# Kernel optimization log

Measured on AMD Instinct MI355X. Metric: run time of the kernel, lower is better.

The kernel has to match this reference:

```python
import jax, jax.numpy as jnp
import numpy as np

B, L, D = 64, 512, 128  # batch, word_len, dim


def setup_inputs() -> dict:
    key = jax.random.key(0)
    ks = jax.random.split(key, 12)
    p = lambda k, s: jax.random.normal(k, s, dtype=jnp.float32) * 0.05
    return {
        "EW": jax.random.normal(ks[0], (B, L, D), dtype=jnp.float32),
        "ES": jax.random.normal(ks[1], (B, L, D), dtype=jnp.float32),
        "WQ_w": p(ks[2], (D, D)), "WQ_b": p(ks[3], (D,)),
        "WK_w": p(ks[4], (D, D)), "WK_b": p(ks[5], (D,)),
        "UQ_w": p(ks[6], (D, D)), "UQ_b": p(ks[7], (D,)),
        "UK_w": p(ks[8], (D, D)), "UK_b": p(ks[9], (D,)),
        "V_w": p(ks[10], (D, D)), "V_b": p(ks[11], (D,)),
    }


def reference(EW, ES, WQ_w, WQ_b, WK_w, WK_b, UQ_w, UQ_b, UK_w, UK_b, V_w, V_b):
    dim = EW.shape[-1]
    word_len = EW.shape[-2]
    scale = 1.0 / (2.0 * dim ** 0.5)
    # word-level Q/K and sentence-level UQ/UK projections (torch Linear: x @ W.T + b)
    Q = (EW @ WQ_w.T + WQ_b) * scale   # [B, L, D]
    K = (EW @ WK_w.T + WK_b) * scale   # [B, L, D]
    UQ = (ES @ UQ_w.T + UQ_b) * scale  # [B, L, D]
    UK = (ES @ UK_w.T + UK_b) * scale  # [B, L, D]
    # two-term score matrix [B, L, L]
    alpha = jnp.einsum('bid,bjd->bij', Q, K) + jnp.einsum('bid,bjd->bij', UQ, UK)
    # manual exp/sum softmax exactly as in the source (no max subtraction;
    # denominator is broadcast along axis 1, faithful to unsqueeze(1))
    numerator = jnp.exp(alpha)                      # [B, L, L]
    denominator = numerator.sum(axis=-1)[:, None, :]  # [B, 1, L]
    soft = numerator / denominator                  # [B, L, L]
    value = EW @ V_w.T + V_b                        # [B, L, D]
    # faithful reinterpreting view (NOT a transpose): [B, L, D] -> [B, D, L]
    value = value.reshape(-1, dim, word_len)
    result = value @ soft                           # [B, D, L]
    return result.reshape(-1, word_len, dim)        # [B, L, D]
```

## Files before the change

### kernel.cpp

```cpp
#include <hip/hip_runtime.h>
#include <hip/hip_bf16.h>

#define NB 64
#define NL 512
#define ND 128
#define NK 256

typedef unsigned short ush;
typedef __attribute__((ext_vector_type(8))) short short8;
typedef __attribute__((ext_vector_type(16))) float f32x16;


__device__ __forceinline__ ush f2bs(float f) {
    union { __hip_bfloat16 h; ush u; } cv;
    cv.h = __float2bfloat16(f);
    return cv.u;
}
__device__ __forceinline__ short8 pack_bf8(float4 a, float4 b) {
    short8 r;
    r[0] = (short)f2bs(a.x); r[1] = (short)f2bs(a.y);
    r[2] = (short)f2bs(a.z); r[3] = (short)f2bs(a.w);
    r[4] = (short)f2bs(b.x); r[5] = (short)f2bs(b.y);
    r[6] = (short)f2bs(b.z); r[7] = (short)f2bs(b.w);
    return r;
}
__device__ __forceinline__ f32x16 zero16() {
    f32x16 z = {0.f,0.f,0.f,0.f,0.f,0.f,0.f,0.f,0.f,0.f,0.f,0.f,0.f,0.f,0.f,0.f};
    return z;
}

__global__ __launch_bounds__(256) void wconv_kernel(
    const float* __restrict__ W0, const float* __restrict__ W1,
    const float* __restrict__ W2, const float* __restrict__ W3,
    const float* __restrict__ W4, ush* __restrict__ Wb)
{
    const int m = blockIdx.y;
    const float* W = (m == 0) ? W0 : (m == 1) ? W1 : (m == 2) ? W2 : (m == 3) ? W3 : W4;
    const int e = (blockIdx.x * 256 + threadIdx.x) * 4;
    float4 v = *(const float4*)(W + e);
    ushort4 o;
    o.x = f2bs(v.x); o.y = f2bs(v.y); o.z = f2bs(v.z); o.w = f2bs(v.w);
    *(ushort4*)(Wb + m * 16384 + e) = o;
}

__global__ __launch_bounds__(256) void projqk_kernel(
    const float* __restrict__ EW, const float* __restrict__ ES,
    const ush* __restrict__ Wb,
    const float* __restrict__ b0, const float* __restrict__ b1,
    const float* __restrict__ b2, const float* __restrict__ b3,
    ush* __restrict__ QUf, ush* __restrict__ KUf)
{
    __shared__ ush Tls[4][2048];
    const int f = blockIdx.x;
    const int xcd = f & 7, loc = f >> 3;
    const int rt = xcd * 32 + (loc >> 2);
    const int m  = loc & 3;
    const int tid = threadIdx.x, w = tid >> 6, lane = tid & 63;
    const int l5 = lane & 31, hi = lane >> 5;
    const float* X = (m >= 2) ? ES : EW;
    const int rbase = rt * 128 + w * 32;

    const float* xr = X + (size_t)(rbase + l5) * ND + hi * 8;
    short8 af[8];
    #pragma unroll
    for (int ks = 0; ks < 8; ++ks)
        af[ks] = pack_bf8(*(const float4*)(xr + ks * 16),
                          *(const float4*)(xr + ks * 16 + 4));

    const ush* Wm = Wb + m * 16384;
    const float* Bp = (m == 0) ? b0 : (m == 1) ? b1 : (m == 2) ? b2 : b3;
    const float scl = 0.044194173824159216f;

    char* Tc = (char*)Tls[w];
    ush* dstf = (m == 0 || m == 2) ? QUf : KUf;
    const int ko = (m >= 2) ? 8 : 0;
    const int p_g = rt * 4 + w;

    #pragma unroll
    for (int pass = 0; pass < 2; ++pass) {
        f32x16 acc[2];
        acc[0] = zero16(); acc[1] = zero16();
        #pragma unroll
        for (int ks = 0; ks < 8; ++ks) {
            #pragma unroll
            for (int nbl = 0; nbl < 2; ++nbl) {
                const int nb = pass * 2 + nbl;
                short8 bf_ = *(const short8*)(Wm + (nb * 32 + l5) * 128 + ks * 16 + hi * 8);
                acc[nbl] = __builtin_amdgcn_mfma_f32_32x32x16_bf16(af[ks], bf_, acc[nbl], 0, 0, 0);
            }
        }
        #pragma unroll
        for (int nbl = 0; nbl < 2; ++nbl) {
            const int nb = pass * 2 + nbl;
            float bias = Bp[nb * 32 + l5];
            #pragma unroll
            for (int r6 = 0; r6 < 16; ++r6) {
                int row = (r6 & 3) + 8 * (r6 >> 2) + 4 * hi;
                int boff = row * 128 + (((nbl * 32 + l5) * 2) ^ ((row & 7) << 4));
                *(ush*)(Tc + boff) = f2bs((acc[nbl][r6] + bias) * scl);
            }
        }
        #pragma unroll
        for (int ks8 = 0; ks8 < 4; ++ks8) {
            int boff = l5 * 128 + ((ks8 * 32 + hi * 16) ^ ((l5 & 7) << 4));
            short8 v = *(const short8*)(Tc + boff);
            int ksg = ko + pass * 4 + ks8;
            *(short8*)(dstf + ((size_t)(p_g * 16 + ksg) * 64 + lane) * 8) = v;
        }
    }
}

__global__ __launch_bounds__(256) void projv_kernel(
    const float* __restrict__ EW, const ush* __restrict__ Wb,
    const float* __restrict__ b4, ush* __restrict__ Vbf)
{
    __shared__ ush lds[16384];
    const int f = blockIdx.x;
    const int rt = (f & 7) * 32 + (f >> 3);
    const int tid = threadIdx.x, w = tid >> 6, lane = tid & 63;
    const int l5 = lane & 31, hi = lane >> 5;
    const int rbase = rt * 128 + w * 32;

    const float* xr = EW + (size_t)(rbase + l5) * ND + hi * 8;
    short8 af[8];
    #pragma unroll
    for (int ks = 0; ks < 8; ++ks)
        af[ks] = pack_bf8(*(const float4*)(xr + ks * 16),
                          *(const float4*)(xr + ks * 16 + 4));

    const ush* Wm = Wb + 4 * 16384;
    f32x16 acc[4];
    acc[0] = zero16(); acc[1] = zero16(); acc[2] = zero16(); acc[3] = zero16();
    #pragma unroll
    for (int ks = 0; ks < 8; ++ks) {
        #pragma unroll
        for (int nb = 0; nb < 4; ++nb) {
            short8 bf_ = *(const short8*)(Wm + (nb * 32 + l5) * 128 + ks * 16 + hi * 8);
            acc[nb] = __builtin_amdgcn_mfma_f32_32x32x16_bf16(af[ks], bf_, acc[nb], 0, 0, 0);
        }
    }

    char* Lc = (char*)lds;
    #pragma unroll
    for (int nb = 0; nb < 4; ++nb) {
        float bias = b4[nb * 32 + l5];
        #pragma unroll
        for (int r6 = 0; r6 < 16; ++r6) {
            int row5 = (r6 & 3) + 8 * (r6 >> 2) + 4 * hi;
            int dl = w * 8 + (row5 >> 2);
            int lcol = (row5 & 3) * 128 + nb * 32 + l5;
            int boff = dl * 1024 + ((lcol * 2) ^ ((dl & 7) << 4));
            *(ush*)(Lc + boff) = f2bs(acc[nb][r6] + bias);
        }
    }
    __syncthreads();
    #pragma unroll
    for (int it = 0; it < 8; ++it) {
        int chunk = it * 256 + tid;
        int ks = chunk >> 6, ln = chunk & 63;
        int l5b = ln & 31, hib = ln >> 5;
        int boff = l5b * 1024 + ((ks * 32 + hib * 16) ^ ((l5b & 7) << 4));
        short8 v = *(const short8*)(Lc + boff);
        *(short8*)(Vbf + ((size_t)(rt * 32 + ks) * 64 + ln) * 8) = v;
    }
}

__global__ __launch_bounds__(256) void alpha_kernel(
    const ush* __restrict__ QUf, const ush* __restrict__ KUf,
    ush* __restrict__ Nf, float* __restrict__ dPart)
{
    __shared__ float red[4][2][16];
    __shared__ ush TlsA[4][2048];
    const int f = blockIdx.x;
    const int xcd = f & 7, loc = f >> 3;
    const int b  = xcd * 8 + (loc >> 5);
    const int rt = (loc >> 1) & 15;
    const int ch = loc & 1;
    const int tid = threadIdx.x, w = tid >> 6, lane = tid & 63;
    const int l5 = lane & 31, hi = lane >> 5;
    const ush* Qb = QUf + (size_t)b * 131072;
    const ush* Kb = KUf + (size_t)b * 131072;
    ush* Nfb = Nf + (size_t)b * 262144;

    const ush* qp = Qb + (size_t)rt * 8192 + lane * 8;
    const int cpg0 = ch * 8 + w * 2;

    f32x16 a0[2], a1[2];
    a0[0] = zero16(); a0[1] = zero16(); a1[0] = zero16(); a1[1] = zero16();
    #pragma unroll
    for (int ks = 0; ks < 16; ks += 2) {
        short8 aqa = *(const short8*)(qp + ks * 512);
        short8 aqb = *(const short8*)(qp + (ks + 1) * 512);
        #pragma unroll
        for (int cp = 0; cp < 2; ++cp) {
            const ush* kp = Kb + (size_t)((cpg0 + cp) * 16) * 512 + lane * 8;
            a0[cp] = __builtin_amdgcn_mfma_f32_32x32x16_bf16(aqa,
                         *(const short8*)(kp + ks * 512), a0[cp], 0, 0, 0);
            a1[cp] = __builtin_amdgcn_mfma_f32_32x32x16_bf16(aqb,
                         *(const short8*)(kp + (ks + 1) * 512), a1[cp], 0, 0, 0);
        }
    }

    float rs[16];
    #pragma unroll
    for (int r6 = 0; r6 < 16; ++r6) rs[r6] = 0.f;
    char* Tc = (char*)TlsA[w];
    #pragma unroll
    for (int cp = 0; cp < 2; ++cp) {
        const int cpg = cpg0 + cp;
        float e[16];
        #pragma unroll
        for (int r6 = 0; r6 < 16; ++r6) {
            e[r6] = __expf(a0[cp][r6] + a1[cp][r6]);
            rs[r6] += e[r6];
        }
        #pragma unroll
        for (int q = 0; q < 8; ++q) {
            int r6 = q * 2;
            int r = (r6 & 3) + 8 * (r6 >> 2) + 4 * hi;
            unsigned int pk = (unsigned int)f2bs(e[r6])
                            | ((unsigned int)f2bs(e[r6 + 1]) << 16);
            *(unsigned int*)(Tc + l5 * 128 + ((r * 2) ^ ((l5 & 7) << 4))) = pk;
        }
        #pragma unroll
        for (int ksl = 0; ksl < 2; ++ksl) {
            short8 v = *(const short8*)(Tc + l5 * 128 +
                           (((ksl * 16 + hi * 8) * 2) ^ ((l5 & 7) << 4)));
            int ksg = rt * 2 + ksl;
            *(short8*)(Nfb + ((size_t)(cpg * 32 + ksg) * 64 + lane) * 8) = v;
        }
    }

    #pragma unroll
    for (int mk = 1; mk <= 16; mk <<= 1)
        #pragma unroll
        for (int r6 = 0; r6 < 16; ++r6) rs[r6] += __shfl_xor(rs[r6], mk, 32);
    if (l5 == 0)
        #pragma unroll
        for (int r6 = 0; r6 < 16; ++r6) red[w][hi][r6] = rs[r6];
    __syncthreads();
    if (tid < 32) {
        int t = tid;
        int hh = (t >> 2) & 1, r6 = (t & 3) + 4 * (t >> 3);
        float s = red[0][hh][r6] + red[1][hh][r6] + red[2][hh][r6] + red[3][hh][r6];
        dPart[((size_t)b * 2 + ch) * NL + rt * 32 + t] = s;
    }
}

__global__ __launch_bounds__(256) void pv_kernel(
    const ush* __restrict__ Vbf, const ush* __restrict__ Nf,
    const float* __restrict__ dPart, float* __restrict__ out)
{
    const int f = blockIdx.x;
    const int xcd = f & 7, loc = f >> 3;
    const int b  = xcd * 8 + (loc >> 4);
    const int ct = loc & 15;
    const int tid = threadIdx.x, w = tid >> 6, lane = tid & 63;
    const int l5 = lane & 31, hi = lane >> 5;
    const ush* Vbb = Vbf + (size_t)b * 65536;
    const ush* Nfb = Nf + (size_t)b * 262144;
    const size_t obase = (size_t)b * (ND * NL);

    const ush* vp = Vbb + (size_t)w * 16384 + lane * 8;
    const ush* np = Nfb + (size_t)ct * 16384 + lane * 8;

    f32x16 acc0 = zero16(), acc1 = zero16();
    #pragma unroll
    for (int ks = 0; ks < 32; ks += 2) {
        acc0 = __builtin_amdgcn_mfma_f32_32x32x16_bf16(*(const short8*)(vp + ks * 512),
                   *(const short8*)(np + ks * 512), acc0, 0, 0, 0);
        acc1 = __builtin_amdgcn_mfma_f32_32x32x16_bf16(*(const short8*)(vp + (ks + 1) * 512),
                   *(const short8*)(np + (ks + 1) * 512), acc1, 0, 0, 0);
    }
    f32x16 acc = acc0 + acc1;
    const int c0 = ct * 32;
    float rd = 1.0f / (dPart[((size_t)b * 2 + 0) * NL + c0 + l5]
                     + dPart[((size_t)b * 2 + 1) * NL + c0 + l5]);
    #pragma unroll
    for (int r6 = 0; r6 < 16; ++r6) {
        int d = w * 32 + (r6 & 3) + 8 * (r6 >> 2) + 4 * hi;
        out[obase + (size_t)d * NL + c0 + l5] = acc[r6] * rd;
    }
}

__global__ __launch_bounds__(256) void fused_kernel(
    const ush* __restrict__ QUf, const ush* __restrict__ KUf,
    const ush* __restrict__ Vbf, float* __restrict__ out)
{
    __shared__ ush Pt2[32 * 136];
    __shared__ float red[128];
    __shared__ float rdenS[32];
    const int f = blockIdx.x;
    const int xcd = f & 7, loc = f >> 3;
    const int b  = xcd * 8 + (loc >> 4);
    const int ct = loc & 15, c0 = ct * 32;
    const int tid = threadIdx.x, w = tid >> 6, lane = tid & 63;
    const int l5 = lane & 31, hi = lane >> 5;
    const ush* Qb  = QUf + (size_t)b * 131072;
    const ush* Kb  = KUf + (size_t)b * 131072;
    const ush* Vbb = Vbf + (size_t)b * 65536;
    const size_t obase = (size_t)b * (ND * NL);

    {
        short8 aq[16];
        const ush* qp = Qb + (size_t)ct * 8192 + lane * 8;
        #pragma unroll
        for (int ks = 0; ks < 16; ++ks) aq[ks] = *(const short8*)(qp + ks * 512);
        float rs[16];
        #pragma unroll
        for (int r = 0; r < 16; ++r) rs[r] = 0.f;
        #pragma unroll
        for (int t = 0; t < 4; ++t) {
            const ush* kp = Kb + (size_t)(w * 4 + t) * 8192 + lane * 8;
            f32x16 a0 = zero16(), a1 = zero16();
            #pragma unroll
            for (int ks = 0; ks < 16; ks += 2) {
                a0 = __builtin_amdgcn_mfma_f32_32x32x16_bf16(aq[ks],     *(const short8*)(kp + ks * 512),       a0, 0, 0, 0);
                a1 = __builtin_amdgcn_mfma_f32_32x32x16_bf16(aq[ks + 1], *(const short8*)(kp + (ks + 1) * 512), a1, 0, 0, 0);
            }
            #pragma unroll
            for (int r = 0; r < 16; ++r) rs[r] += __expf(a0[r] + a1[r]);
        }
        #pragma unroll
        for (int mk = 1; mk <= 16; mk <<= 1)
            #pragma unroll
            for (int r = 0; r < 16; ++r) rs[r] += __shfl_xor(rs[r], mk, 32);
        if (l5 == 0)
            #pragma unroll
            for (int r = 0; r < 16; ++r) red[(w * 2 + hi) * 16 + r] = rs[r];
    }
    __syncthreads();
    if (tid < 32) {
        int c = tid;
        int h2 = (c >> 2) & 1, r = (c & 3) + 4 * (c >> 3);
        float s = 0.f;
        #pragma unroll
        for (int kh = 0; kh < 4; ++kh) s += red[(kh * 2 + h2) * 16 + r];
        rdenS[c] = 1.0f / s;
    }
    __syncthreads();

    const int p2 = w;
    const float rden = rdenS[l5];
    const ush* kp2 = Kb + (size_t)ct * 8192 + lane * 8;
    f32x16 oA = zero16(), oB = zero16();

    for (int it = 0; it < 4; ++it) {
        if (it) __syncthreads();
        const ush* qp2 = Qb + (size_t)(it * 4 + p2) * 8192 + lane * 8;
        f32x16 s0 = zero16(), s1 = zero16();
        #pragma unroll
        for (int ks = 0; ks < 16; ks += 2) {
            s0 = __builtin_amdgcn_mfma_f32_32x32x16_bf16(*(const short8*)(qp2 + ks * 512),
                                                         *(const short8*)(kp2 + ks * 512),       s0, 0, 0, 0);
            s1 = __builtin_amdgcn_mfma_f32_32x32x16_bf16(*(const short8*)(qp2 + (ks + 1) * 512),
                                                         *(const short8*)(kp2 + (ks + 1) * 512), s1, 0, 0, 0);
        }
        #pragma unroll
        for (int q = 0; q < 4; ++q) {
            ushort4 pv;
            pv.x = f2bs(__expf(s0[q * 4 + 0] + s1[q * 4 + 0]) * rden);
            pv.y = f2bs(__expf(s0[q * 4 + 1] + s1[q * 4 + 1]) * rden);
            pv.z = f2bs(__expf(s0[q * 4 + 2] + s1[q * 4 + 2]) * rden);
            pv.w = f2bs(__expf(s0[q * 4 + 3] + s1[q * 4 + 3]) * rden);
            int boff = l5 * 272 + (((p2 * 32 + q * 8 + hi * 4) * 2) ^ ((l5 & 7) << 4));
            *(ushort4*)((char*)Pt2 + boff) = pv;
        }
        __syncthreads();
        #pragma unroll
        for (int j = 0; j < 8; j += 2) {
            short8 va0 = *(const short8*)(Vbb + ((size_t)(p2 * 32 + it * 8 + j) * 64 + lane) * 8);
            short8 pb0 = *(const short8*)((char*)Pt2 + l5 * 272 + (((j * 16 + hi * 8) * 2) ^ ((l5 & 7) << 4)));
            oA = __builtin_amdgcn_mfma_f32_32x32x16_bf16(va0, pb0, oA, 0, 0, 0);
            short8 va1 = *(const short8*)(Vbb + ((size_t)(p2 * 32 + it * 8 + j + 1) * 64 + lane) * 8);
            short8 pb1 = *(const short8*)((char*)Pt2 + l5 * 272 + ((((j + 1) * 16 + hi * 8) * 2) ^ ((l5 & 7) << 4)));
            oB = __builtin_amdgcn_mfma_f32_32x32x16_bf16(va1, pb1, oB, 0, 0, 0);
        }
    }
    f32x16 oacc = oA + oB;
    #pragma unroll
    for (int r = 0; r < 16; ++r) {
        int d = p2 * 32 + (r & 3) + 8 * (r >> 2) + 4 * hi;
        out[obase + (size_t)d * NL + c0 + l5] = oacc[r];
    }
}

extern "C" void kernel_launch(void* const* d_in, const int* in_sizes, int n_in,
                              void* d_out, int out_size, void* d_ws, size_t ws_size,
                              hipStream_t stream)
{
    const float* EW   = (const float*)d_in[0];
    const float* ES   = (const float*)d_in[1];
    const float* WQ_w = (const float*)d_in[2];
    const float* WQ_b = (const float*)d_in[3];
    const float* WK_w = (const float*)d_in[4];
    const float* WK_b = (const float*)d_in[5];
    const float* UQ_w = (const float*)d_in[6];
    const float* UQ_b = (const float*)d_in[7];
    const float* UK_w = (const float*)d_in[8];
    const float* UK_b = (const float*)d_in[9];
    const float* V_w  = (const float*)d_in[10];
    const float* V_b  = (const float*)d_in[11];

    if (ws_size < (size_t)41 * 1024 * 1024) return;

    char* ws = (char*)d_ws;
    ush* QUf = (ush*)ws;
    ush* KUf = (ush*)(ws + (size_t)16 * 1024 * 1024);
    ush* Vbf = (ush*)(ws + (size_t)32 * 1024 * 1024);
    ush* Wb  = (ush*)(ws + (size_t)40 * 1024 * 1024);
    float* dPart = (float*)(ws + (size_t)40 * 1024 * 1024 + 512 * 1024);
    ush* Nf  = (ush*)(ws + (size_t)41 * 1024 * 1024);
    float* outp = (float*)d_out;

    wconv_kernel<<<dim3(16, 5), 256, 0, stream>>>(WQ_w, WK_w, UQ_w, UK_w, V_w, Wb);
    projqk_kernel<<<1024, 256, 0, stream>>>(EW, ES, Wb,
                                            WQ_b, WK_b, UQ_b, UK_b, QUf, KUf);
    projv_kernel<<<256, 256, 0, stream>>>(EW, Wb, V_b, Vbf);
    if (ws_size >= (size_t)74 * 1024 * 1024) {
        alpha_kernel<<<2048, 256, 0, stream>>>(QUf, KUf, Nf, dPart);
        pv_kernel<<<1024, 256, 0, stream>>>(Vbf, Nf, dPart, outp);
    } else {
        fused_kernel<<<1024, 256, 0, stream>>>(QUf, KUf, Vbf, outp);
    }
}
```

Measured before the change: 80.54 us.

## Store Q/K projections in FP8 and compute scores with FP8 MFMA

The projection kernel now writes Q/UQ and K/UK as FP8 (e4m3) rather than bf16. It uses a larger pre-scale and folds the remaining 1/256 factor into the exponent argument. The alpha kernel uses the fp8 32x32x16 MFMA with 8-byte operand loads. This halves the Q/K traffic and uses the faster fp8 matrix path. The cost is lower precision in the score matrix, which feeds an exponential without max subtraction and can amplify error. The fused fallback kernel is removed, and the launcher now requires the larger workspace.

```diff
diff --git a/kernel.cpp b/kernel.cpp
--- a/kernel.cpp
+++ b/kernel.cpp
@@ -15,6 +15,11 @@
     union { __hip_bfloat16 h; ush u; } cv;
     cv.h = __float2bfloat16(f);
     return cv.u;
+}
+__device__ __forceinline__ float bs2f(ush u) {
+    union { unsigned int i; float f; } cv;
+    cv.i = ((unsigned int)u) << 16;
+    return cv.f;
 }
 __device__ __forceinline__ short8 pack_bf8(float4 a, float4 b) {
     short8 r;
@@ -48,7 +53,7 @@
     const ush* __restrict__ Wb,
     const float* __restrict__ b0, const float* __restrict__ b1,
     const float* __restrict__ b2, const float* __restrict__ b3,
-    ush* __restrict__ QUf, ush* __restrict__ KUf)
+    char* __restrict__ QUf, char* __restrict__ KUf)
 {
     __shared__ ush Tls[4][2048];
     const int f = blockIdx.x;
@@ -69,10 +74,10 @@
 
     const ush* Wm = Wb + m * 16384;
     const float* Bp = (m == 0) ? b0 : (m == 1) ? b1 : (m == 2) ? b2 : b3;
-    const float scl = 0.044194173824159216f;
+    const float scl = 0.70710678118654752f;
 
     char* Tc = (char*)Tls[w];
-    ush* dstf = (m == 0 || m == 2) ? QUf : KUf;
+    char* dstf = (m == 0 || m == 2) ? QUf : KUf;
     const int ko = (m >= 2) ? 8 : 0;
     const int p_g = rt * 4 + w;
 
@@ -104,8 +109,16 @@
         for (int ks8 = 0; ks8 < 4; ++ks8) {
             int boff = l5 * 128 + ((ks8 * 32 + hi * 16) ^ ((l5 & 7) << 4));
             short8 v = *(const short8*)(Tc + boff);
+            float fv[8];
+            #pragma unroll
+            for (int e = 0; e < 8; ++e) fv[e] = bs2f((ush)v[e]);
+            int dw0 = __builtin_amdgcn_cvt_pk_fp8_f32(fv[0], fv[1], 0, 0);
+            dw0     = __builtin_amdgcn_cvt_pk_fp8_f32(fv[2], fv[3], dw0, 1);
+            int dw1 = __builtin_amdgcn_cvt_pk_fp8_f32(fv[4], fv[5], 0, 0);
+            dw1     = __builtin_amdgcn_cvt_pk_fp8_f32(fv[6], fv[7], dw1, 1);
             int ksg = ko + pass * 4 + ks8;
-            *(short8*)(dstf + ((size_t)(p_g * 16 + ksg) * 64 + lane) * 8) = v;
+            int2 st; st.x = dw0; st.y = dw1;
+            *(int2*)(dstf + ((size_t)(p_g * 16 + ksg) * 64 + lane) * 8) = st;
         }
     }
 }
@@ -166,7 +179,7 @@
 }
 
 __global__ __launch_bounds__(256) void alpha_kernel(
-    const ush* __restrict__ QUf, const ush* __restrict__ KUf,
+    const char* __restrict__ QUf, const char* __restrict__ KUf,
     ush* __restrict__ Nf, float* __restrict__ dPart)
 {
     __shared__ float red[4][2][16];
@@ -178,27 +191,29 @@
     const int ch = loc & 1;
     const int tid = threadIdx.x, w = tid >> 6, lane = tid & 63;
     const int l5 = lane & 31, hi = lane >> 5;
-    const ush* Qb = QUf + (size_t)b * 131072;
-    const ush* Kb = KUf + (size_t)b * 131072;
+    const char* Qb = QUf + (size_t)b * 131072;
+    const char* Kb = KUf + (size_t)b * 131072;
     ush* Nfb = Nf + (size_t)b * 262144;
 
-    const ush* qp = Qb + (size_t)rt * 8192 + lane * 8;
+    const char* qp = Qb + (size_t)rt * 8192 + lane * 8;
     const int cpg0 = ch * 8 + w * 2;
+    const char* kp0 = Kb + (size_t)(cpg0 + 0) * 8192 + lane * 8;
+    const char* kp1 = Kb + (size_t)(cpg0 + 1) * 8192 + lane * 8;
 
     f32x16 a0[2], a1[2];
     a0[0] = zero16(); a0[1] = zero16(); a1[0] = zero16(); a1[1] = zero16();
     #pragma unroll
     for (int ks = 0; ks < 16; ks += 2) {
-        short8 aqa = *(const short8*)(qp + ks * 512);
-        short8 aqb = *(const short8*)(qp + (ks + 1) * 512);
-        #pragma unroll
-        for (int cp = 0; cp < 2; ++cp) {
-            const ush* kp = Kb + (size_t)((cpg0 + cp) * 16) * 512 + lane * 8;
-            a0[cp] = __builtin_amdgcn_mfma_f32_32x32x16_bf16(aqa,
-                         *(const short8*)(kp + ks * 512), a0[cp], 0, 0, 0);
-            a1[cp] = __builtin_amdgcn_mfma_f32_32x32x16_bf16(aqb,
-                         *(const short8*)(kp + (ks + 1) * 512), a1[cp], 0, 0, 0);
-        }
+        long aqa = *(const long*)(qp + ks * 512);
+        long aqb = *(const long*)(qp + (ks + 1) * 512);
+        a0[0] = __builtin_amdgcn_mfma_f32_32x32x16_fp8_fp8(aqa,
+                    *(const long*)(kp0 + ks * 512), a0[0], 0, 0, 0);
+        a1[0] = __builtin_amdgcn_mfma_f32_32x32x16_fp8_fp8(aqb,
+                    *(const long*)(kp0 + (ks + 1) * 512), a1[0], 0, 0, 0);
+        a0[1] = __builtin_amdgcn_mfma_f32_32x32x16_fp8_fp8(aqa,
+                    *(const long*)(kp1 + ks * 512), a0[1], 0, 0, 0);
+        a1[1] = __builtin_amdgcn_mfma_f32_32x32x16_fp8_fp8(aqb,
+                    *(const long*)(kp1 + (ks + 1) * 512), a1[1], 0, 0, 0);
     }
 
     float rs[16];
@@ -211,7 +226,7 @@
         float e[16];
         #pragma unroll
         for (int r6 = 0; r6 < 16; ++r6) {
-            e[r6] = __expf(a0[cp][r6] + a1[cp][r6]);
+            e[r6] = __expf((a0[cp][r6] + a1[cp][r6]) * 0.00390625f);
             rs[r6] += e[r6];
         }
         #pragma unroll
@@ -280,108 +295,6 @@
     for (int r6 = 0; r6 < 16; ++r6) {
         int d = w * 32 + (r6 & 3) + 8 * (r6 >> 2) + 4 * hi;
         out[obase + (size_t)d * NL + c0 + l5] = acc[r6] * rd;
-    }
-}
-
-__global__ __launch_bounds__(256) void fused_kernel(
-    const ush* __restrict__ QUf, const ush* __restrict__ KUf,
-    const ush* __restrict__ Vbf, float* __restrict__ out)
-{
-    __shared__ ush Pt2[32 * 136];
-    __shared__ float red[128];
-    __shared__ float rdenS[32];
-    const int f = blockIdx.x;
-    const int xcd = f & 7, loc = f >> 3;
-    const int b  = xcd * 8 + (loc >> 4);
-    const int ct = loc & 15, c0 = ct * 32;
-    const int tid = threadIdx.x, w = tid >> 6, lane = tid & 63;
-    const int l5 = lane & 31, hi = lane >> 5;
-    const ush* Qb  = QUf + (size_t)b * 131072;
-    const ush* Kb  = KUf + (size_t)b * 131072;
-    const ush* Vbb = Vbf + (size_t)b * 65536;
-    const size_t obase = (size_t)b * (ND * NL);
-
-    {
-        short8 aq[16];
-        const ush* qp = Qb + (size_t)ct * 8192 + lane * 8;
-        #pragma unroll
-        for (int ks = 0; ks < 16; ++ks) aq[ks] = *(const short8*)(qp + ks * 512);
-        float rs[16];
-        #pragma unroll
-        for (int r = 0; r < 16; ++r) rs[r] = 0.f;
-        #pragma unroll
-        for (int t = 0; t < 4; ++t) {
-            const ush* kp = Kb + (size_t)(w * 4 + t) * 8192 + lane * 8;
-            f32x16 a0 = zero16(), a1 = zero16();
-            #pragma unroll
-            for (int ks = 0; ks < 16; ks += 2) {
-                a0 = __builtin_amdgcn_mfma_f32_32x32x16_bf16(aq[ks],     *(const short8*)(kp + ks * 512),       a0, 0, 0, 0);
-                a1 = __builtin_amdgcn_mfma_f32_32x32x16_bf16(aq[ks + 1], *(const short8*)(kp + (ks + 1) * 512), a1, 0, 0, 0);
-            }
-            #pragma unroll
-            for (int r = 0; r < 16; ++r) rs[r] += __expf(a0[r] + a1[r]);
-        }
-        #pragma unroll
-        for (int mk = 1; mk <= 16; mk <<= 1)
-            #pragma unroll
-            for (int r = 0; r < 16; ++r) rs[r] += __shfl_xor(rs[r], mk, 32);
-        if (l5 == 0)
-            #pragma unroll
-            for (int r = 0; r < 16; ++r) red[(w * 2 + hi) * 16 + r] = rs[r];
-    }
-    __syncthreads();
-    if (tid < 32) {
-        int c = tid;
-        int h2 = (c >> 2) & 1, r = (c & 3) + 4 * (c >> 3);
-        float s = 0.f;
-        #pragma unroll
-        for (int kh = 0; kh < 4; ++kh) s += red[(kh * 2 + h2) * 16 + r];
-        rdenS[c] = 1.0f / s;
-    }
-    __syncthreads();
-
-    const int p2 = w;
-    const float rden = rdenS[l5];
-    const ush* kp2 = Kb + (size_t)ct * 8192 + lane * 8;
-    f32x16 oA = zero16(), oB = zero16();
-
-    for (int it = 0; it < 4; ++it) {
-        if (it) __syncthreads();
-        const ush* qp2 = Qb + (size_t)(it * 4 + p2) * 8192 + lane * 8;
-        f32x16 s0 = zero16(), s1 = zero16();
-        #pragma unroll
-        for (int ks = 0; ks < 16; ks += 2) {
-            s0 = __builtin_amdgcn_mfma_f32_32x32x16_bf16(*(const short8*)(qp2 + ks * 512),
-                                                         *(const short8*)(kp2 + ks * 512),       s0, 0, 0, 0);
-            s1 = __builtin_amdgcn_mfma_f32_32x32x16_bf16(*(const short8*)(qp2 + (ks + 1) * 512),
-                                                         *(const short8*)(kp2 + (ks + 1) * 512), s1, 0, 0, 0);
-        }
-        #pragma unroll
-        for (int q = 0; q < 4; ++q) {
-            ushort4 pv;
-            pv.x = f2bs(__expf(s0[q * 4 + 0] + s1[q * 4 + 0]) * rden);
-            pv.y = f2bs(__expf(s0[q * 4 + 1] + s1[q * 4 + 1]) * rden);
-            pv.z = f2bs(__expf(s0[q * 4 + 2] + s1[q * 4 + 2]) * rden);
-            pv.w = f2bs(__expf(s0[q * 4 + 3] + s1[q * 4 + 3]) * rden);
-            int boff = l5 * 272 + (((p2 * 32 + q * 8 + hi * 4) * 2) ^ ((l5 & 7) << 4));
-            *(ushort4*)((char*)Pt2 + boff) = pv;
-        }
-        __syncthreads();
-        #pragma unroll
-        for (int j = 0; j < 8; j += 2) {
-            short8 va0 = *(const short8*)(Vbb + ((size_t)(p2 * 32 + it * 8 + j) * 64 + lane) * 8);
-            short8 pb0 = *(const short8*)((char*)Pt2 + l5 * 272 + (((j * 16 + hi * 8) * 2) ^ ((l5 & 7) << 4)));
-            oA = __builtin_amdgcn_mfma_f32_32x32x16_bf16(va0, pb0, oA, 0, 0, 0);
-            short8 va1 = *(const short8*)(Vbb + ((size_t)(p2 * 32 + it * 8 + j + 1) * 64 + lane) * 8);
-            short8 pb1 = *(const short8*)((char*)Pt2 + l5 * 272 + ((((j + 1) * 16 + hi * 8) * 2) ^ ((l5 & 7) << 4)));
-            oB = __builtin_amdgcn_mfma_f32_32x32x16_bf16(va1, pb1, oB, 0, 0, 0);
-        }
-    }
-    f32x16 oacc = oA + oB;
-    #pragma unroll
-    for (int r = 0; r < 16; ++r) {
-        int d = p2 * 32 + (r & 3) + 8 * (r >> 2) + 4 * hi;
-        out[obase + (size_t)d * NL + c0 + l5] = oacc[r];
     }
 }
 
@@ -402,25 +315,21 @@
     const float* V_w  = (const float*)d_in[10];
     const float* V_b  = (const float*)d_in[11];
 
-    if (ws_size < (size_t)41 * 1024 * 1024) return;
+    if (ws_size < (size_t)74 * 1024 * 1024) return;
 
     char* ws = (char*)d_ws;
-    ush* QUf = (ush*)ws;
-    ush* KUf = (ush*)(ws + (size_t)16 * 1024 * 1024);
-    ush* Vbf = (ush*)(ws + (size_t)32 * 1024 * 1024);
-    ush* Wb  = (ush*)(ws + (size_t)40 * 1024 * 1024);
+    char* QUf = ws;
+    char* KUf = ws + (size_t)16 * 1024 * 1024;
+    ush*  Vbf = (ush*)(ws + (size_t)32 * 1024 * 1024);
+    ush*  Wb  = (ush*)(ws + (size_t)40 * 1024 * 1024);
     float* dPart = (float*)(ws + (size_t)40 * 1024 * 1024 + 512 * 1024);
-    ush* Nf  = (ush*)(ws + (size_t)41 * 1024 * 1024);
+    ush*  Nf  = (ush*)(ws + (size_t)41 * 1024 * 1024);
     float* outp = (float*)d_out;
 
     wconv_kernel<<<dim3(16, 5), 256, 0, stream>>>(WQ_w, WK_w, UQ_w, UK_w, V_w, Wb);
     projqk_kernel<<<1024, 256, 0, stream>>>(EW, ES, Wb,
                                             WQ_b, WK_b, UQ_b, UK_b, QUf, KUf);
     projv_kernel<<<256, 256, 0, stream>>>(EW, Wb, V_b, Vbf);
-    if (ws_size >= (size_t)74 * 1024 * 1024) {
-        alpha_kernel<<<2048, 256, 0, stream>>>(QUf, KUf, Nf, dPart);
-        pv_kernel<<<1024, 256, 0, stream>>>(Vbf, Nf, dPart, outp);
-    } else {
-        fused_kernel<<<1024, 256, 0, stream>>>(QUf, KUf, Vbf, outp);
-    }
-}
+    alpha_kernel<<<2048, 256, 0, stream>>>(QUf, KUf, Nf, dPart);
+    pv_kernel<<<1024, 256, 0, stream>>>(Vbf, Nf, dPart, outp);
+}
```

Measured after the change: 76.88 us (median of 3 runs). 1.05x faster.
